# Kernel tuning notes

Hardware: AMD Instinct MI355X
Metric: run time of the kernel (lower is better)

Reference implementation:

```python
import jax, jax.numpy as jnp
import numpy as np

L = 128  # side_len
B = 16   # batch of poses


def setup_inputs() -> dict:
    key = jax.random.key(0)
    k1, k2 = jax.random.split(key)
    rotmat = jax.random.normal(k1, (B, 3, 3), dtype=jnp.float32)
    vol = jax.random.normal(k2, (L, L, L), dtype=jnp.float32) * 0.1
    # buffer 'coords_<scale>': meshgrid of linspace(-1,1,L), stacked as [y,x,z]
    lin = jnp.linspace(-1.0, 1.0, L, dtype=jnp.float32)
    X, Y, Z = jnp.meshgrid(lin, lin, lin, indexing='ij')
    coords = jnp.stack([Y, X, Z], axis=-1).reshape(-1, 3)  # [L^3, 3]
    return {"rotmat": rotmat, "vol": vol, "coords": coords, "proj_axis": 3}


def _grid_sample_3d(vol, pts):
    """torch grid_sample (trilinear, align_corners=True, zeros padding).
    vol: [L,L,L] laid out (D,H,W); pts: [B,N,3] with last dim (x,y,z) in [-1,1],
    x indexing W (last vol dim), y indexing H, z indexing D."""
    Ld = vol.shape[0]
    idx = (pts + 1.0) * 0.5 * (Ld - 1)  # align_corners=True mapping
    x, y, z = idx[..., 0], idx[..., 1], idx[..., 2]
    x0 = jnp.floor(x); y0 = jnp.floor(y); z0 = jnp.floor(z)
    wx1 = x - x0; wy1 = y - y0; wz1 = z - z0
    wx0 = 1.0 - wx1; wy0 = 1.0 - wy1; wz0 = 1.0 - wz1
    x0i = x0.astype(jnp.int32); y0i = y0.astype(jnp.int32); z0i = z0.astype(jnp.int32)
    x1i = x0i + 1; y1i = y0i + 1; z1i = z0i + 1

    def gather(zi, yi, xi):
        valid = ((xi >= 0) & (xi < Ld) & (yi >= 0) & (yi < Ld)
                 & (zi >= 0) & (zi < Ld))
        v = vol[jnp.clip(zi, 0, Ld - 1), jnp.clip(yi, 0, Ld - 1),
                jnp.clip(xi, 0, Ld - 1)]
        return jnp.where(valid, v, 0.0)

    return (gather(z0i, y0i, x0i) * wz0 * wy0 * wx0
            + gather(z0i, y0i, x1i) * wz0 * wy0 * wx1
            + gather(z0i, y1i, x0i) * wz0 * wy1 * wx0
            + gather(z0i, y1i, x1i) * wz0 * wy1 * wx1
            + gather(z1i, y0i, x0i) * wz1 * wy0 * wx0
            + gather(z1i, y0i, x1i) * wz1 * wy0 * wx1
            + gather(z1i, y1i, x0i) * wz1 * wy1 * wx0
            + gather(z1i, y1i, x1i) * wz1 * wy1 * wx1)


def reference(rotmat, vol, coords, proj_axis):
    # pytorch3d Rotate.transform_points: row vectors -> points @ R
    pts = jnp.einsum('nj,bjk->bnk', coords, rotmat)       # [B, L^3, 3]
    rot_vol = _grid_sample_3d(vol, pts)                    # [B, L^3]
    Ld = vol.shape[-1]
    proj = rot_vol.reshape(-1, Ld, Ld, Ld).sum(axis=proj_axis)  # [B, L, L]
    return proj[:, None, :, :]                             # [B, 1, L, L]
```

## Files before the change

kernel.cpp:

```cpp
#include <hip/hip_runtime.h>
#include <hip/hip_fp16.h>

#define LSIDE 128
#define NB 16

union P8 { __half h[8]; int4 v; };

__global__ __launch_bounds__(256) void pack8_kernel(
    const float* __restrict__ vol, int4* __restrict__ packed)
{
    const int t = blockIdx.x * 256 + threadIdx.x;
    const int x = t & 127;
    const int y = (t >> 7) & 127;
    const int z = t >> 14;
    const int xp = min(x + 1, 127);
    const int yp = min(y + 1, 127);
    const int zp = min(z + 1, 127);
    const float* p00 = vol + (z  * LSIDE + y ) * LSIDE;
    const float* p01 = vol + (z  * LSIDE + yp) * LSIDE;
    const float* p10 = vol + (zp * LSIDE + y ) * LSIDE;
    const float* p11 = vol + (zp * LSIDE + yp) * LSIDE;
    P8 o;
    o.h[0] = __float2half(p00[x]); o.h[1] = __float2half(p00[xp]);
    o.h[2] = __float2half(p01[x]); o.h[3] = __float2half(p01[xp]);
    o.h[4] = __float2half(p10[x]); o.h[5] = __float2half(p10[xp]);
    o.h[6] = __float2half(p11[x]); o.h[7] = __float2half(p11[xp]);
    packed[t] = o.v;
}

__device__ __forceinline__ void clip1(float r, float c, float A, float B,
                                      float& lo, float& hi)
{
    if (fabsf(r) > 1e-12f) {
        const float inv = 1.0f / r;
        const float a = (A - c) * inv, e = (B - c) * inv;
        lo = fmaxf(lo, fminf(a, e));
        hi = fminf(hi, fmaxf(a, e));
    } else if (c < A || c > B) {
        lo = 1e9f; hi = -1e9f;
    }
}

__device__ __forceinline__ void axis_fix(float g, int& c, float& w0, float& w1)
{
    const float f = floorf(g);
    const int x0 = (int)f;
    const float t1 = g - f;
    const float t0 = 1.0f - t1;
    w0 = ((unsigned)x0 <= 127u) ? t0 : ((x0 == -1) ? t1 : 0.0f);
    w1 = ((unsigned)x0 <= 126u) ? t1 : 0.0f;
    c = min(max(x0, 0), LSIDE - 1);
}

__global__ __launch_bounds__(256) void ProjectorMultiRes_59236188947236_kernel(
    const float* __restrict__ rotmat,
    const int4* __restrict__ packed,
    const float* __restrict__ coords,
    float* __restrict__ out)
{
    __shared__ float lin[LSIDE];
    __shared__ float red[LSIDE];
    const int tid = threadIdx.x;
    if (tid < LSIDE) lin[tid] = coords[3 * tid + 2];
    __syncthreads();

    const int logical = (blockIdx.x & 7) * 256 + (blockIdx.x >> 3);
    const int b = logical >> 7;
    const int i = logical & 127;
    const int j = tid & 127;
    const int half = tid >> 7;

    const float* R = rotmat + b * 9;
    const float r00 = R[0], r01 = R[1], r02 = R[2];
    const float r10 = R[3], r11 = R[4], r12 = R[5];
    const float r20 = R[6], r21 = R[7], r22 = R[8];

    const float lj = lin[j];
    const float li = lin[i];
    const float bx = lj * r00 + li * r10;
    const float by = lj * r01 + li * r11;
    const float bz = lj * r02 + li * r12;

    const float h = 2.0f / 127.0f;

    const float Bd = 1.0f + 1.0f / 63.5f + 1e-4f;
    float lo = -1.0f, hi = 1.0f;
    clip1(r20, bx, -Bd, Bd, lo, hi);
    clip1(r21, by, -Bd, Bd, lo, hi);
    clip1(r22, bz, -Bd, Bd, lo, hi);
    int k0 = max((int)ceilf((lo + 1.0f) / h) - 1, 0);
    int k1 = min((int)floorf((hi + 1.0f) / h) + 2, LSIDE);
    if (k1 < k0) k1 = k0;

    const float dxg = h * r20 * 63.5f;
    const float dyg = h * r21 * 63.5f;
    const float dzg = h * r22 * 63.5f;

    const int cnt  = k1 - k0;
    const int kmid = k0 + ((cnt + 1) >> 1);
    const int ks = half ? kmid : k0;
    const int ke = half ? k1   : kmid;

    float gx = fmaf(fmaf((float)ks, h, -1.0f), r20, bx) * 63.5f + 63.5f;
    float gy = fmaf(fmaf((float)ks, h, -1.0f), r21, by) * 63.5f + 63.5f;
    float gz = fmaf(fmaf((float)ks, h, -1.0f), r22, bz) * 63.5f + 63.5f;

    float acc = 0.0f;

    #pragma unroll 2
    for (int k = ks; k < ke; ++k) {
        int cx, cy, cz;
        float w0x, w1x, w0y, w1y, w0z, w1z;
        axis_fix(gx, cx, w0x, w1x);
        axis_fix(gy, cy, w0y, w1y);
        axis_fix(gz, cz, w0z, w1z);

        P8 c;
        c.v = packed[(cz * LSIDE + cy) * LSIDE + cx];
        gx += dxg; gy += dyg; gz += dzg;

        const float v000 = __half2float(c.h[0]);
        const float v001 = __half2float(c.h[1]);
        const float v010 = __half2float(c.h[2]);
        const float v011 = __half2float(c.h[3]);
        const float v100 = __half2float(c.h[4]);
        const float v101 = __half2float(c.h[5]);
        const float v110 = __half2float(c.h[6]);
        const float v111 = __half2float(c.h[7]);
        acc += ((v000 * w0x + v001 * w1x) * w0y + (v010 * w0x + v011 * w1x) * w1y) * w0z
             + ((v100 * w0x + v101 * w1x) * w0y + (v110 * w0x + v111 * w1x) * w1y) * w1z;
    }

    if (half) red[j] = acc;
    __syncthreads();
    if (!half) out[(b * LSIDE + i) * LSIDE + j] = acc + red[j];
}

extern "C" void kernel_launch(void* const* d_in, const int* in_sizes, int n_in,
                              void* d_out, int out_size, void* d_ws, size_t ws_size,
                              hipStream_t stream) {
    const float* rotmat = (const float*)d_in[0];
    const float* vol    = (const float*)d_in[1];
    const float* coords = (const float*)d_in[2];
    float* out = (float*)d_out;

    int4* packed = (int4*)d_ws;
    pack8_kernel<<<(LSIDE * LSIDE * LSIDE) / 256, 256, 0, stream>>>(vol, packed);
    ProjectorMultiRes_59236188947236_kernel<<<NB * LSIDE, 256, 0, stream>>>(
        rotmat, packed, coords, out);
}
```

Before: 92.21 us.

## Split each ray across 8 lanes with interleaved steps and shuffle reduction

Each output pixel's ray is now marched by 8 adjacent lanes, each taking every 8th sample, instead of two half-blocks splitting the range. Partial sums are combined with width-8 shuffles, which removes the shared-memory reduction and the block barriers. Blocks now cover 32 pixels of a row, so the grid has four times as many blocks. The intent is better load balance and more memory parallelism, at the cost of less gather locality per lane and redundant per-pixel setup across the 8 lanes.

New measurement: 89.18 us. 3.3% less time.

```diff
diff --git a/kernel.cpp b/kernel.cpp
--- a/kernel.cpp
+++ b/kernel.cpp
@@ -58,25 +58,26 @@
     const float* __restrict__ coords,
     float* __restrict__ out)
 {
-    __shared__ float lin[LSIDE];
-    __shared__ float red[LSIDE];
-    const int tid = threadIdx.x;
-    if (tid < LSIDE) lin[tid] = coords[3 * tid + 2];
-    __syncthreads();
+    const int tid  = threadIdx.x;
+    const int wid  = tid >> 6;
+    const int lane = tid & 63;
+    const int g    = lane >> 3;
+    const int l    = lane & 7;
 
-    const int logical = (blockIdx.x & 7) * 256 + (blockIdx.x >> 3);
-    const int b = logical >> 7;
-    const int i = logical & 127;
-    const int j = tid & 127;
-    const int half = tid >> 7;
+    const int logical = (blockIdx.x & 7) * 1024 + (blockIdx.x >> 3);
+    const int b   = logical >> 9;
+    const int rem = logical & 511;
+    const int i   = rem >> 2;
+    const int jc  = rem & 3;
+    const int j   = jc * 32 + wid * 8 + g;
 
     const float* R = rotmat + b * 9;
     const float r00 = R[0], r01 = R[1], r02 = R[2];
     const float r10 = R[3], r11 = R[4], r12 = R[5];
     const float r20 = R[6], r21 = R[7], r22 = R[8];
 
-    const float lj = lin[j];
-    const float li = lin[i];
+    const float lj = coords[3 * j + 2];
+    const float li = coords[3 * i + 2];
     const float bx = lj * r00 + li * r10;
     const float by = lj * r01 + li * r11;
     const float bz = lj * r02 + li * r12;
@@ -95,20 +96,18 @@
     const float dxg = h * r20 * 63.5f;
     const float dyg = h * r21 * 63.5f;
     const float dzg = h * r22 * 63.5f;
+    const float sdx = 8.0f * dxg, sdy = 8.0f * dyg, sdz = 8.0f * dzg;
 
-    const int cnt  = k1 - k0;
-    const int kmid = k0 + ((cnt + 1) >> 1);
-    const int ks = half ? kmid : k0;
-    const int ke = half ? k1   : kmid;
-
-    float gx = fmaf(fmaf((float)ks, h, -1.0f), r20, bx) * 63.5f + 63.5f;
-    float gy = fmaf(fmaf((float)ks, h, -1.0f), r21, by) * 63.5f + 63.5f;
-    float gz = fmaf(fmaf((float)ks, h, -1.0f), r22, bz) * 63.5f + 63.5f;
+    int k = k0 + l;
+    const float lk = fmaf((float)k, h, -1.0f);
+    float gx = fmaf(lk, r20, bx) * 63.5f + 63.5f;
+    float gy = fmaf(lk, r21, by) * 63.5f + 63.5f;
+    float gz = fmaf(lk, r22, bz) * 63.5f + 63.5f;
 
     float acc = 0.0f;
 
     #pragma unroll 2
-    for (int k = ks; k < ke; ++k) {
+    for (; k < k1; k += 8) {
         int cx, cy, cz;
         float w0x, w1x, w0y, w1y, w0z, w1z;
         axis_fix(gx, cx, w0x, w1x);
@@ -117,7 +116,7 @@
 
         P8 c;
         c.v = packed[(cz * LSIDE + cy) * LSIDE + cx];
-        gx += dxg; gy += dyg; gz += dzg;
+        gx += sdx; gy += sdy; gz += sdz;
 
         const float v000 = __half2float(c.h[0]);
         const float v001 = __half2float(c.h[1]);
@@ -131,9 +130,11 @@
              + ((v100 * w0x + v101 * w1x) * w0y + (v110 * w0x + v111 * w1x) * w1y) * w1z;
     }
 
-    if (half) red[j] = acc;
-    __syncthreads();
-    if (!half) out[(b * LSIDE + i) * LSIDE + j] = acc + red[j];
+    acc += __shfl_down(acc, 4, 8);
+    acc += __shfl_down(acc, 2, 8);
+    acc += __shfl_down(acc, 1, 8);
+    if (l == 0)
+        out[(b * LSIDE + i) * LSIDE + j] = acc;
 }
 
 extern "C" void kernel_launch(void* const* d_in, const int* in_sizes, int n_in,
@@ -146,6 +147,6 @@
 
     int4* packed = (int4*)d_ws;
     pack8_kernel<<<(LSIDE * LSIDE * LSIDE) / 256, 256, 0, stream>>>(vol, packed);
-    ProjectorMultiRes_59236188947236_kernel<<<NB * LSIDE, 256, 0, stream>>>(
+    ProjectorMultiRes_59236188947236_kernel<<<NB * LSIDE * LSIDE / 32, 256, 0, stream>>>(
         rotmat, packed, coords, out);
 }
```
